# Performance work log

Measured on AMD Instinct MI355X. Metric: run time of the kernel, lower is better.

## Reference

```python
import jax, jax.numpy as jnp
import numpy as np

B_, T_, D_MODEL = 2, 1024, 1024
D_STATE, D_CONV, EXPAND = 16, 4, 2
D_INNER = D_MODEL * EXPAND


def setup_inputs() -> dict:
    key = jax.random.key(0)
    ks = jax.random.split(key, 12)
    def s(k, shape, sc=0.02):
        return jax.random.normal(k, shape, jnp.float32) * sc
    return {
        "x": jax.random.normal(ks[0], (B_, T_, D_MODEL), jnp.float32),
        "ln_g": jnp.ones((D_MODEL,), jnp.float32),
        "ln_b": jnp.zeros((D_MODEL,), jnp.float32),
        "W_in": s(ks[1], (D_MODEL, 2 * D_INNER)),
        "b_in": s(ks[2], (2 * D_INNER,)),
        "conv_w": s(ks[3], (D_INNER, 1, D_CONV)),  # depthwise kernel, torch OIH layout
        "conv_b": s(ks[4], (D_INNER,)),
        "A": s(ks[5], (D_INNER, D_STATE), 0.1),
        "W_B": s(ks[6], (D_INNER, D_STATE)),
        "b_B": s(ks[7], (D_STATE,)),
        "W_C": s(ks[8], (D_INNER, D_STATE)),
        "b_C": s(ks[9], (D_STATE,)),
        "D": jnp.ones((D_INNER,), jnp.float32),
        "W_out": s(ks[10], (D_INNER, D_MODEL)),
        "b_out": s(ks[11], (D_MODEL,)),
    }


def _ssm_forward(x, ln_g, ln_b, W_in, b_in, conv_w, conv_b, A, W_B, b_B, W_C, b_C, D, W_out, b_out):
    eps = 1e-5
    # LayerNorm (biased variance, as in torch)
    mu = jnp.mean(x, axis=-1, keepdims=True)
    var = jnp.var(x, axis=-1, keepdims=True)
    xn = (x - mu) / jnp.sqrt(var + eps) * ln_g + ln_b
    # in_proj -> split into x path and gate
    proj = xn @ W_in + b_in                      # (b, t, 2*d_inner)
    xp, gate = jnp.split(proj, 2, axis=-1)
    # depthwise causal conv1d (padding=d_conv-1 on the left == torch pad + truncate)
    xc = jax.lax.conv_general_dilated(
        xp.transpose(0, 2, 1), conv_w,
        window_strides=(1,), padding=[(D_CONV - 1, 0)],
        dimension_numbers=("NCH", "OIH", "NCH"),
        feature_group_count=D_INNER,
    ).transpose(0, 2, 1) + conv_b                # (b, t, d_inner)
    xc = jax.nn.silu(xc)
    Bt = xc @ W_B + b_B                          # (b, t, d_state)
    Ct = xc @ W_C + b_C                          # (b, t, d_state)
    a = jax.nn.sigmoid(A)                        # (d_inner, d_state), per-channel decay
    u = Bt[:, :, None, :] * xc[:, :, :, None]    # (b, t, d_inner, d_state)
    a_full = jnp.broadcast_to(a, u.shape)
    # h_t = a * h_{t-1} + u_t  via first-order-recurrence associative scan
    def combine(c1, c2):
        a1, u1 = c1
        a2, u2 = c2
        return a2 * a1, a2 * u1 + u2
    _, h = jax.lax.associative_scan(combine, (a_full, u), axis=1)
    y = jnp.einsum("btns,bts->btn", h, Ct) + D * xc
    y = y * jax.nn.silu(gate)
    return y @ W_out + b_out + x                 # residual (dropout is identity in eval)


def reference(x, ln_g, ln_b, W_in, b_in, conv_w, conv_b, A, W_B, b_B, W_C, b_C, D, W_out, b_out):
    return _ssm_forward(x, ln_g, ln_b, W_in, b_in, conv_w, conv_b, A, W_B, b_B, W_C, b_C, D, W_out, b_out)
```

## Files before the change

kernel.cpp:

```cpp
#include <hip/hip_runtime.h>
#include <hip/hip_bf16.h>
#include <stdint.h>

using u16 = unsigned short;
typedef short bf16x8 __attribute__((ext_vector_type(8)));
typedef float f32x4 __attribute__((ext_vector_type(4)));

__device__ __forceinline__ float b2f(u16 u) {
  union { unsigned int i; float f; } v; v.i = ((unsigned int)u) << 16; return v.f;
}
__device__ __forceinline__ u16 f2b(float f) {
  __hip_bfloat16 h = __float2bfloat16(f);
  u16 r; __builtin_memcpy(&r, &h, 2); return r;
}
__device__ __forceinline__ bool probe_bf16(const void* p) {
  return *(const unsigned int*)p == 0x3F803F80u;
}
__device__ __forceinline__ float loadf(const void* p, size_t i, bool bf) {
  return bf ? b2f(((const u16*)p)[i]) : ((const float*)p)[i];
}
__device__ __forceinline__ void gload_lds16(const u16* g, u16* l) {
  __builtin_amdgcn_global_load_lds(
      (const __attribute__((address_space(1))) unsigned int*)(g),
      (__attribute__((address_space(3))) unsigned int*)(l),
      16, 0, 0);
}
template <int BK>
__device__ __forceinline__ int swkey(int row) {
  if constexpr (BK == 32) return (row >> 1) & 3;
  else return row & (BK / 8 - 1);
}

__device__ __forceinline__ void do_transpose(const void* __restrict__ in, u16* __restrict__ out,
                                             int R, int C, int bx, int by, int tid, bool bf) {
  __shared__ u16 tile[32][33];
  int c0 = bx * 32, r0 = by * 32;
  int tx = tid & 31, ty = tid >> 5;
#pragma unroll
  for (int i = 0; i < 4; i++) {
    size_t idx = (size_t)(r0 + ty + i * 8) * C + c0 + tx;
    tile[ty + i * 8][tx] = bf ? ((const u16*)in)[idx] : f2b(((const float*)in)[idx]);
  }
  __syncthreads();
#pragma unroll
  for (int i = 0; i < 4; i++)
    out[(size_t)(c0 + ty + i * 8) * R + r0 + tx] = tile[tx][ty + i * 8];
}

__launch_bounds__(256)
__global__ void prep_kernel(const void* __restrict__ W_in, u16* __restrict__ WinT,
                            const void* __restrict__ W_out, u16* __restrict__ WoutT,
                            const void* __restrict__ WB, const void* __restrict__ WC,
                            u16* __restrict__ WTbc, const void* __restrict__ probe) {
  const bool bf = probe_bf16(probe);
  const int bid = blockIdx.x, tid = threadIdx.x;
  if (bid < 4096) {
    do_transpose(W_in, WinT, 1024, 4096, bid & 127, bid >> 7, tid, bf);
  } else if (bid < 6144) {
    int b2 = bid - 4096;
    do_transpose(W_out, WoutT, 2048, 1024, b2 & 31, b2 >> 5, tid, bf);
  } else {
    int g = (bid - 6144) * 256 + tid;
    int c = g >> 8, k0 = (g & 255) * 8;
    const void* W = (c < 16) ? WB : WC;
    int cc = c & 15;
    u16 pk[8];
#pragma unroll
    for (int e = 0; e < 8; e++)
      pk[e] = bf ? ((const u16*)W)[(size_t)(k0 + e) * 16 + cc]
                 : f2b(((const float*)W)[(size_t)(k0 + e) * 16 + cc]);
    *(int4*)(WTbc + (size_t)c * 2048 + k0) = *(int4*)pk;
  }
}

__launch_bounds__(256)
__global__ void ln_kernel(const void* __restrict__ x, const void* __restrict__ g,
                          const void* __restrict__ b, u16* __restrict__ xn) {
  const bool bf = probe_bf16(g);
  const int row = blockIdx.x, tid = threadIdx.x;
  const size_t base = (size_t)row * 1024;
  float v[4]; float s = 0.f, s2 = 0.f;
#pragma unroll
  for (int i = 0; i < 4; i++) {
    v[i] = loadf(x, base + tid + i * 256, bf);
    s += v[i]; s2 += v[i] * v[i];
  }
#pragma unroll
  for (int m = 32; m >= 1; m >>= 1) { s += __shfl_xor(s, m); s2 += __shfl_xor(s2, m); }
  __shared__ float rs[4], rs2[4];
  if ((tid & 63) == 0) { rs[tid >> 6] = s; rs2[tid >> 6] = s2; }
  __syncthreads();
  s = rs[0] + rs[1] + rs[2] + rs[3];
  s2 = rs2[0] + rs2[1] + rs2[2] + rs2[3];
  float mu = s * (1.f / 1024.f);
  float var = s2 * (1.f / 1024.f) - mu * mu;
  float rstd = rsqrtf(var + 1e-5f);
#pragma unroll
  for (int i = 0; i < 4; i++) {
    int c = tid + i * 256;
    float o = (v[i] - mu) * rstd * loadf(g, c, bf) + loadf(b, c, bf);
    xn[base + c] = f2b(o);
  }
}

template <int ROWS, int BK>
__device__ __forceinline__ void stage_tile(const u16* __restrict__ g, u16* lbuf,
                                           int K, int wave, int lane) {
  constexpr int LPR = BK / 8;
  constexpr int RPI = 512 / BK;
  constexpr int NI = ROWS / RPI;
  const int lr = lane / LPR, lc = lane % LPR;
#pragma unroll
  for (int j = wave; j < NI; j += 4) {
    int row = j * RPI + lr;
    int col = (lc ^ swkey<BK>(row)) * 8;
    gload_lds16(g + (size_t)row * K + col, lbuf + (size_t)j * RPI * BK);
  }
}

template <int BM, int BN, int BK, bool RESID, bool DUALOUT, bool PARTIAL>
__launch_bounds__(256)
__global__ void gemm_async(const u16* __restrict__ A, const u16* __restrict__ BT,
                           const void* __restrict__ bias, const void* __restrict__ resid,
                           void* __restrict__ Cout, float* __restrict__ Cpart,
                           int M, int N, int K, int k_len,
                           const void* __restrict__ probe) {
  constexpr int WM = BM / 2, WN = BN / 2;
  constexpr int TM = WM / 16, TN = WN / 16;
  constexpr int KF = BK / 32;
  __shared__ __align__(16) u16 lds[2][(BM + BN) * BK];
  const int tid = threadIdx.x;
  const int bm = blockIdx.x, bn = blockIdx.y, bz = blockIdx.z;
  const int lane = tid & 63, wave = tid >> 6;
  const int wm = wave >> 1, wn = wave & 1;
  const int lrow = lane & 15, quad = lane >> 4;
  f32x4 acc[TM][TN] = {};
  const u16* Ag = A + (size_t)bm * BM * K + (size_t)bz * k_len;
  const u16* Bg = BT + (size_t)bn * BN * K + (size_t)bz * k_len;

  stage_tile<BM, BK>(Ag, &lds[0][0], K, wave, lane);
  stage_tile<BN, BK>(Bg, &lds[0][BM * BK], K, wave, lane);
  __syncthreads();

  int cur = 0;
  for (int k0 = 0; k0 < k_len; k0 += BK, cur ^= 1) {
    if (k0 + BK < k_len) {
      stage_tile<BM, BK>(Ag + k0 + BK, &lds[cur ^ 1][0], K, wave, lane);
      stage_tile<BN, BK>(Bg + k0 + BK, &lds[cur ^ 1][BM * BK], K, wave, lane);
    }
    const u16* bufA = &lds[cur][0];
    const u16* bufB = &lds[cur][BM * BK];
#pragma unroll
    for (int f = 0; f < KF; f++) {
      bf16x8 af[TM], bv[TN];
#pragma unroll
      for (int i = 0; i < TM; i++) {
        int row = wm * WM + i * 16 + lrow;
        af[i] = *(const bf16x8*)&bufA[(size_t)row * BK + (((f * 4 + quad) ^ swkey<BK>(row)) * 8)];
      }
#pragma unroll
      for (int j = 0; j < TN; j++) {
        int row = wn * WN + j * 16 + lrow;
        bv[j] = *(const bf16x8*)&bufB[(size_t)row * BK + (((f * 4 + quad) ^ swkey<BK>(row)) * 8)];
      }
#pragma unroll
      for (int i = 0; i < TM; i++)
#pragma unroll
        for (int j = 0; j < TN; j++)
          acc[i][j] = __builtin_amdgcn_mfma_f32_16x16x32_bf16(af[i], bv[j], acc[i][j], 0, 0, 0);
    }
    __syncthreads();
  }

  if constexpr (PARTIAL) {
    float* P = Cpart + (size_t)bz * M * N;
#pragma unroll
    for (int i = 0; i < TM; i++)
#pragma unroll
      for (int j = 0; j < TN; j++) {
        int col = bn * BN + wn * WN + j * 16 + lrow;
#pragma unroll
        for (int r = 0; r < 4; r++) {
          int row = bm * BM + wm * WM + i * 16 + quad * 4 + r;
          P[(size_t)row * N + col] = acc[i][j][r];
        }
      }
    return;
  }

  const bool bf = probe_bf16(probe);
#pragma unroll
  for (int i = 0; i < TM; i++) {
#pragma unroll
    for (int j = 0; j < TN; j++) {
      int col = bn * BN + wn * WN + j * 16 + lrow;
      float bvv = loadf(bias, col, bf);
#pragma unroll
      for (int r = 0; r < 4; r++) {
        int row = bm * BM + wm * WM + i * 16 + quad * 4 + r;
        float v = acc[i][j][r] + bvv;
        if constexpr (RESID) v += loadf(resid, (size_t)row * N + col, bf);
        if constexpr (DUALOUT) {
          if (bf) ((u16*)Cout)[(size_t)row * N + col] = f2b(v);
          else    ((float*)Cout)[(size_t)row * N + col] = v;
        } else {
          ((u16*)Cout)[(size_t)row * N + col] = f2b(v);
        }
      }
    }
  }
}

__launch_bounds__(256)
__global__ void reduce_out(const float* __restrict__ p, const void* __restrict__ bias,
                           const void* __restrict__ resid, void* __restrict__ out,
                           const void* __restrict__ probe) {
  const bool bf = probe_bf16(probe);
  const int row = blockIdx.x, c0 = threadIdx.x * 4;
  const size_t i = (size_t)row * 1024 + c0;
  f32x4 a = *(const f32x4*)(p + i);
  f32x4 b = *(const f32x4*)(p + (size_t)2048 * 1024 + i);
  float o[4];
#pragma unroll
  for (int e = 0; e < 4; e++)
    o[e] = a[e] + b[e] + loadf(bias, c0 + e, bf) + loadf(resid, i + e, bf);
  if (bf) {
    u16 pk[4];
#pragma unroll
    for (int e = 0; e < 4; e++) pk[e] = f2b(o[e]);
    *(uint2*)((u16*)out + i) = *(uint2*)pk;
  } else {
    f32x4 v; v[0] = o[0]; v[1] = o[1]; v[2] = o[2]; v[3] = o[3];
    *(f32x4*)((float*)out + i) = v;
  }
}

__global__ void conv_silu_kernel(const u16* __restrict__ proj, const void* __restrict__ cw,
                                 const void* __restrict__ cb, u16* __restrict__ xc,
                                 const void* __restrict__ probe) {
  const bool bf = probe_bf16(probe);
  const int n = blockIdx.x * 256 + threadIdx.x;
  const int row = blockIdx.y;
  const int t = row & 1023;
  float w[4];
#pragma unroll
  for (int k = 0; k < 4; k++) w[k] = loadf(cw, n * 4 + k, bf);
  float s = loadf(cb, n, bf);
#pragma unroll
  for (int k = 0; k < 4; k++) {
    int tt = t - 3 + k;
    if (tt >= 0) s += b2f(proj[(size_t)(row - 3 + k) * 4096 + n]) * w[k];
  }
  float sg = 1.f / (1.f + __expf(-s));
  xc[(size_t)row * 2048 + n] = f2b(s * sg);
}

__launch_bounds__(256)
__global__ void gemm_bc(const u16* __restrict__ A, const u16* __restrict__ WT,
                        float* __restrict__ part) {
  constexpr int BK = 64, KLEN = 128;
  __shared__ __align__(16) u16 lds[2][(128 + 32) * BK];
  const int tid = threadIdx.x;
  const int bm = blockIdx.x, bz = blockIdx.y;
  const int lane = tid & 63, wave = tid >> 6;
  const int lrow = lane & 15, quad = lane >> 4;
  f32x4 acc[2][2] = {};
  const u16* Ag = A + (size_t)bm * 128 * 2048 + bz * KLEN;
  const u16* Bg = WT + bz * KLEN;

  stage_tile<128, BK>(Ag, &lds[0][0], 2048, wave, lane);
  stage_tile<32, BK>(Bg, &lds[0][128 * BK], 2048, wave, lane);
  __syncthreads();
  int cur = 0;
  for (int k0 = 0; k0 < KLEN; k0 += BK, cur ^= 1) {
    if (k0 + BK < KLEN) {
      stage_tile<128, BK>(Ag + k0 + BK, &lds[cur ^ 1][0], 2048, wave, lane);
      stage_tile<32, BK>(Bg + k0 + BK, &lds[cur ^ 1][128 * BK], 2048, wave, lane);
    }
    const u16* bufA = &lds[cur][0];
    const u16* bufB = &lds[cur][128 * BK];
#pragma unroll
    for (int f = 0; f < 2; f++) {
      bf16x8 af[2], bv[2];
#pragma unroll
      for (int i = 0; i < 2; i++) {
        int row = wave * 32 + i * 16 + lrow;
        af[i] = *(const bf16x8*)&bufA[(size_t)row * BK + (((f * 4 + quad) ^ (row & 7)) * 8)];
      }
#pragma unroll
      for (int j = 0; j < 2; j++) {
        int row = j * 16 + lrow;
        bv[j] = *(const bf16x8*)&bufB[(size_t)row * BK + (((f * 4 + quad) ^ (row & 7)) * 8)];
      }
#pragma unroll
      for (int i = 0; i < 2; i++)
#pragma unroll
        for (int j = 0; j < 2; j++)
          acc[i][j] = __builtin_amdgcn_mfma_f32_16x16x32_bf16(af[i], bv[j], acc[i][j], 0, 0, 0);
    }
    __syncthreads();
  }
#pragma unroll
  for (int i = 0; i < 2; i++)
#pragma unroll
    for (int j = 0; j < 2; j++) {
      int col = j * 16 + lrow;
#pragma unroll
      for (int r = 0; r < 4; r++) {
        int row = bm * 128 + wave * 32 + i * 16 + quad * 4 + r;
        part[((size_t)bz * 2048 + row) * 32 + col] = acc[i][j][r];
      }
    }
}

__launch_bounds__(256)
__global__ void reduce_bc(const float* __restrict__ part, const void* __restrict__ bB,
                          const void* __restrict__ bC, float* __restrict__ BC,
                          const void* __restrict__ probe) {
  const bool bf = probe_bf16(probe);
  const int g = blockIdx.x * 256 + threadIdx.x;
  const int c = g & 31;
  float s = (c < 16) ? loadf(bB, c, bf) : loadf(bC, c - 16, bf);
#pragma unroll
  for (int z = 0; z < 16; z++) s += part[(size_t)z * 65536 + g];
  BC[g] = s;
}

__launch_bounds__(256)
__global__ void scan_pass1(const u16* __restrict__ xc, const float* __restrict__ BC,
                           const void* __restrict__ Abuf, float* __restrict__ carry,
                           const void* __restrict__ probe) {
  const bool bf = probe_bf16(probe);
  const int tid = threadIdx.x;
  const int c = blockIdx.x & 31, ng = (blockIdx.x >> 5) & 7, bi = blockIdx.x >> 8;
  const int n = ng * 256 + tid;
  float a[16], h[16];
#pragma unroll
  for (int s = 0; s < 16; s++) {
    float av = loadf(Abuf, n * 16 + s, bf);
    a[s] = 1.f / (1.f + __expf(-av));
    h[s] = 0.f;
  }
  __shared__ __align__(16) u16 xs[32 * 256];
  __shared__ __align__(16) float bcs[32 * 32];
  const u16* xcp = xc + (size_t)bi * 1024 * 2048 + ng * 256;
  const float* bcp = BC + (size_t)bi * 1024 * 32;
  const int tc = c * 32;
#pragma unroll
  for (int i = 0; i < 4; i++) {
    int ch = tid + i * 256;
    int r = ch >> 5, cv = (ch & 31) * 8;
    *(int4*)&xs[ch * 8] = *(const int4*)(xcp + (size_t)(tc + r) * 2048 + cv);
  }
  {
    int r = tid >> 3, cv = (tid & 7) * 4;
    *(int4*)&bcs[tid * 4] = *(const int4*)(bcp + (size_t)(tc + r) * 32 + cv);
  }
  __syncthreads();
  for (int t = 0; t < 32; t++) {
    float x = b2f(xs[t * 256 + tid]);
#pragma unroll
    for (int s = 0; s < 16; s++)
      h[s] = __builtin_fmaf(a[s], h[s], bcs[t * 32 + s] * x);
  }
  float* cp = carry + ((size_t)(bi * 32 + c) * 2048 + n) * 16;
#pragma unroll
  for (int s = 0; s < 16; s++) cp[s] = h[s];
}

__launch_bounds__(256)
__global__ void scan_prefix(float* __restrict__ carry, const void* __restrict__ Abuf,
                            const void* __restrict__ probe) {
  const bool bf = probe_bf16(probe);
  const int g = blockIdx.x * 256 + threadIdx.x;
  const int s = g & 15, n = (g >> 4) & 2047, bi = g >> 15;
  float a = 1.f / (1.f + __expf(-loadf(Abuf, n * 16 + s, bf)));
  float aL = a;
#pragma unroll
  for (int i = 0; i < 5; i++) aL = aL * aL;
  float running = 0.f;
  for (int c = 0; c < 32; c++) {
    size_t idx = ((size_t)(bi * 32 + c) * 2048 + n) * 16 + s;
    float tmp = carry[idx];
    carry[idx] = running;
    running = __builtin_fmaf(aL, running, tmp);
  }
}

__launch_bounds__(256)
__global__ void scan_pass2(const u16* __restrict__ xc, const u16* __restrict__ proj,
                           const float* __restrict__ BC, const void* __restrict__ Abuf,
                           const void* __restrict__ Dbuf, const float* __restrict__ carry,
                           u16* __restrict__ ybar, const void* __restrict__ probe) {
  const bool bf = probe_bf16(probe);
  const int tid = threadIdx.x;
  const int c = blockIdx.x & 31, ng = (blockIdx.x >> 5) & 7, bi = blockIdx.x >> 8;
  const int n = ng * 256 + tid;
  float a[16], h[16];
  const float* cp = carry + ((size_t)(bi * 32 + c) * 2048 + n) * 16;
#pragma unroll
  for (int s = 0; s < 16; s++) {
    float av = loadf(Abuf, n * 16 + s, bf);
    a[s] = 1.f / (1.f + __expf(-av));
    h[s] = cp[s];
  }
  const float Dn = loadf(Dbuf, n, bf);
  __shared__ __align__(16) u16 xs[32 * 256];
  __shared__ __align__(16) u16 gs[32 * 256];
  __shared__ __align__(16) float bcs[32 * 32];
  const u16* xcp = xc + (size_t)bi * 1024 * 2048 + ng * 256;
  const u16* gp = proj + (size_t)bi * 1024 * 4096 + 2048 + ng * 256;
  const float* bcp = BC + (size_t)bi * 1024 * 32;
  u16* yp = ybar + (size_t)bi * 1024 * 2048 + ng * 256;
  const int tc = c * 32;
#pragma unroll
  for (int i = 0; i < 4; i++) {
    int ch = tid + i * 256;
    int r = ch >> 5, cv = (ch & 31) * 8;
    *(int4*)&xs[ch * 8] = *(const int4*)(xcp + (size_t)(tc + r) * 2048 + cv);
    *(int4*)&gs[ch * 8] = *(const int4*)(gp + (size_t)(tc + r) * 4096 + cv);
  }
  {
    int r = tid >> 3, cv = (tid & 7) * 4;
    *(int4*)&bcs[tid * 4] = *(const int4*)(bcp + (size_t)(tc + r) * 32 + cv);
  }
  __syncthreads();
  for (int t = 0; t < 32; t++) {
    float x = b2f(xs[t * 256 + tid]);
    float acc = 0.f;
#pragma unroll
    for (int s = 0; s < 16; s++) {
      h[s] = __builtin_fmaf(a[s], h[s], bcs[t * 32 + s] * x);
      acc = __builtin_fmaf(h[s], bcs[t * 32 + 16 + s], acc);
    }
    float y = acc + Dn * x;
    float g = b2f(gs[t * 256 + tid]);
    float yg = y * g / (1.f + __expf(-g));
    yp[(size_t)(tc + t) * 2048 + tid] = f2b(yg);
  }
}

extern "C" void kernel_launch(void* const* d_in, const int* in_sizes, int n_in,
                              void* d_out, int out_size, void* d_ws, size_t ws_size,
                              hipStream_t stream) {
  const void* x = d_in[0];
  const void* ln_g = d_in[1];
  const void* ln_b = d_in[2];
  const void* W_in = d_in[3];
  const void* b_in = d_in[4];
  const void* conv_w = d_in[5];
  const void* conv_b = d_in[6];
  const void* A = d_in[7];
  const void* W_B = d_in[8];
  const void* b_B = d_in[9];
  const void* W_C = d_in[10];
  const void* b_C = d_in[11];
  const void* Dp = d_in[12];
  const void* W_out = d_in[13];
  const void* b_out = d_in[14];
  const void* probe = ln_g;

  char* ws = (char*)d_ws;
  u16* WinT = (u16*)ws;
  u16* ybar = (u16*)ws;
  u16* xn = (u16*)(ws + (size_t)8 * 1024 * 1024);
  u16* proj = (u16*)(ws + (size_t)12 * 1024 * 1024);
  u16* xcb = (u16*)(ws + (size_t)28 * 1024 * 1024);
  float* BC = (float*)(ws + (size_t)36 * 1024 * 1024);
  float* carry = (float*)(ws + (size_t)36 * 1024 * 1024 + 256 * 1024);
  u16* WTbc = (u16*)(ws + (size_t)46 * 1024 * 1024);
  float* part = (float*)(ws + (size_t)48 * 1024 * 1024);
  u16* WoutT = (u16*)(ws + (size_t)64 * 1024 * 1024);
  float* part_bc = (float*)(ws + (size_t)68 * 1024 * 1024);

  prep_kernel<<<6176, 256, 0, stream>>>(W_in, WinT, W_out, WoutT, W_B, W_C, WTbc, probe);
  ln_kernel<<<2048, 256, 0, stream>>>(x, ln_g, ln_b, xn);
  gemm_async<128, 128, 64, false, false, false><<<dim3(16, 32), 256, 0, stream>>>(
      xn, WinT, b_in, nullptr, proj, nullptr, 2048, 4096, 1024, 1024, probe);
  conv_silu_kernel<<<dim3(8, 2048), 256, 0, stream>>>(proj, conv_w, conv_b, xcb, probe);
  gemm_bc<<<dim3(16, 16), 256, 0, stream>>>(xcb, WTbc, part_bc);
  reduce_bc<<<256, 256, 0, stream>>>(part_bc, b_B, b_C, BC, probe);
  scan_pass1<<<512, 256, 0, stream>>>(xcb, BC, A, carry, probe);
  scan_prefix<<<256, 256, 0, stream>>>(carry, A, probe);
  scan_pass2<<<512, 256, 0, stream>>>(xcb, proj, BC, A, Dp, carry, ybar, probe);
  gemm_async<128, 64, 64, false, false, true><<<dim3(16, 16, 2), 256, 0, stream>>>(
      ybar, WoutT, nullptr, nullptr, nullptr, part, 2048, 1024, 2048, 1024, probe);
  reduce_out<<<2048, 256, 0, stream>>>(part, b_out, x, d_out, probe);
}
```

Baseline: 219.3 us.

## Fuse LN into prep, conv into BC GEMM, and scan passes into cooperative kernel

Merges the LayerNorm launch into the weight-prep kernel. The depthwise conv+SiLU is computed inside the B/C projection GEMM, writing xc while also staging it into LDS for the MFMA. The BC partial reduction and the three scan phases (chunk carry, prefix, output) are folded into one cooperative kernel that uses grid-wide syncs. This removes several launches and some global round trips, in exchange for grid-sync overhead and needing all 512 blocks to be co-resident.

Result: slower. 466.9 us (+112.9%).

```diff
diff --git a/kernel.cpp b/kernel.cpp
--- a/kernel.cpp
+++ b/kernel.cpp
@@ -1,6 +1,9 @@
 #include <hip/hip_runtime.h>
 #include <hip/hip_bf16.h>
+#include <hip/hip_cooperative_groups.h>
 #include <stdint.h>
+
+namespace cg = cooperative_groups;
 
 using u16 = unsigned short;
 typedef short bf16x8 __attribute__((ext_vector_type(8)));
@@ -48,20 +51,22 @@
 }
 
 __launch_bounds__(256)
-__global__ void prep_kernel(const void* __restrict__ W_in, u16* __restrict__ WinT,
-                            const void* __restrict__ W_out, u16* __restrict__ WoutT,
-                            const void* __restrict__ WB, const void* __restrict__ WC,
-                            u16* __restrict__ WTbc, const void* __restrict__ probe) {
-  const bool bf = probe_bf16(probe);
+__global__ void prep_ln_kernel(const void* __restrict__ W_in, u16* __restrict__ WinT,
+                               const void* __restrict__ W_out, u16* __restrict__ WoutT,
+                               const void* __restrict__ WB, const void* __restrict__ WC,
+                               u16* __restrict__ WTbc, const void* __restrict__ x,
+                               const void* __restrict__ g, const void* __restrict__ b,
+                               u16* __restrict__ xn) {
+  const bool bf = probe_bf16(g);
   const int bid = blockIdx.x, tid = threadIdx.x;
   if (bid < 4096) {
     do_transpose(W_in, WinT, 1024, 4096, bid & 127, bid >> 7, tid, bf);
   } else if (bid < 6144) {
     int b2 = bid - 4096;
     do_transpose(W_out, WoutT, 2048, 1024, b2 & 31, b2 >> 5, tid, bf);
-  } else {
-    int g = (bid - 6144) * 256 + tid;
-    int c = g >> 8, k0 = (g & 255) * 8;
+  } else if (bid < 6176) {
+    int gg = (bid - 6144) * 256 + tid;
+    int c = gg >> 8, k0 = (gg & 255) * 8;
     const void* W = (c < 16) ? WB : WC;
     int cc = c & 15;
     u16 pk[8];
@@ -70,36 +75,31 @@
       pk[e] = bf ? ((const u16*)W)[(size_t)(k0 + e) * 16 + cc]
                  : f2b(((const float*)W)[(size_t)(k0 + e) * 16 + cc]);
     *(int4*)(WTbc + (size_t)c * 2048 + k0) = *(int4*)pk;
-  }
-}
-
-__launch_bounds__(256)
-__global__ void ln_kernel(const void* __restrict__ x, const void* __restrict__ g,
-                          const void* __restrict__ b, u16* __restrict__ xn) {
-  const bool bf = probe_bf16(g);
-  const int row = blockIdx.x, tid = threadIdx.x;
-  const size_t base = (size_t)row * 1024;
-  float v[4]; float s = 0.f, s2 = 0.f;
-#pragma unroll
-  for (int i = 0; i < 4; i++) {
-    v[i] = loadf(x, base + tid + i * 256, bf);
-    s += v[i]; s2 += v[i] * v[i];
-  }
-#pragma unroll
-  for (int m = 32; m >= 1; m >>= 1) { s += __shfl_xor(s, m); s2 += __shfl_xor(s2, m); }
-  __shared__ float rs[4], rs2[4];
-  if ((tid & 63) == 0) { rs[tid >> 6] = s; rs2[tid >> 6] = s2; }
-  __syncthreads();
-  s = rs[0] + rs[1] + rs[2] + rs[3];
-  s2 = rs2[0] + rs2[1] + rs2[2] + rs2[3];
-  float mu = s * (1.f / 1024.f);
-  float var = s2 * (1.f / 1024.f) - mu * mu;
-  float rstd = rsqrtf(var + 1e-5f);
-#pragma unroll
-  for (int i = 0; i < 4; i++) {
-    int c = tid + i * 256;
-    float o = (v[i] - mu) * rstd * loadf(g, c, bf) + loadf(b, c, bf);
-    xn[base + c] = f2b(o);
+  } else {
+    const int row = bid - 6176;
+    const size_t base = (size_t)row * 1024;
+    float v[4]; float s = 0.f, s2 = 0.f;
+#pragma unroll
+    for (int i = 0; i < 4; i++) {
+      v[i] = loadf(x, base + tid + i * 256, bf);
+      s += v[i]; s2 += v[i] * v[i];
+    }
+#pragma unroll
+    for (int m = 32; m >= 1; m >>= 1) { s += __shfl_xor(s, m); s2 += __shfl_xor(s2, m); }
+    __shared__ float rs[4], rs2[4];
+    if ((tid & 63) == 0) { rs[tid >> 6] = s; rs2[tid >> 6] = s2; }
+    __syncthreads();
+    s = rs[0] + rs[1] + rs[2] + rs[3];
+    s2 = rs2[0] + rs2[1] + rs2[2] + rs2[3];
+    float mu = s * (1.f / 1024.f);
+    float var = s2 * (1.f / 1024.f) - mu * mu;
+    float rstd = rsqrtf(var + 1e-5f);
+#pragma unroll
+    for (int i = 0; i < 4; i++) {
+      int c = tid + i * 256;
+      float o = (v[i] - mu) * rstd * loadf(g, c, bf) + loadf(b, c, bf);
+      xn[base + c] = f2b(o);
+    }
   }
 }
 
@@ -118,12 +118,11 @@
   }
 }
 
-template <int BM, int BN, int BK, bool RESID, bool DUALOUT, bool PARTIAL>
+template <int BM, int BN, int BK, bool PARTIAL>
 __launch_bounds__(256)
 __global__ void gemm_async(const u16* __restrict__ A, const u16* __restrict__ BT,
-                           const void* __restrict__ bias, const void* __restrict__ resid,
-                           void* __restrict__ Cout, float* __restrict__ Cpart,
-                           int M, int N, int K, int k_len,
+                           const void* __restrict__ bias, void* __restrict__ Cout,
+                           float* __restrict__ Cpart, int M, int N, int K, int k_len,
                            const void* __restrict__ probe) {
   constexpr int WM = BM / 2, WN = BN / 2;
   constexpr int TM = WM / 16, TN = WN / 16;
@@ -198,14 +197,7 @@
 #pragma unroll
       for (int r = 0; r < 4; r++) {
         int row = bm * BM + wm * WM + i * 16 + quad * 4 + r;
-        float v = acc[i][j][r] + bvv;
-        if constexpr (RESID) v += loadf(resid, (size_t)row * N + col, bf);
-        if constexpr (DUALOUT) {
-          if (bf) ((u16*)Cout)[(size_t)row * N + col] = f2b(v);
-          else    ((float*)Cout)[(size_t)row * N + col] = v;
-        } else {
-          ((u16*)Cout)[(size_t)row * N + col] = f2b(v);
-        }
+        ((u16*)Cout)[(size_t)row * N + col] = f2b(acc[i][j][r] + bvv);
       }
     }
   }
@@ -235,70 +227,79 @@
   }
 }
 
-__global__ void conv_silu_kernel(const u16* __restrict__ proj, const void* __restrict__ cw,
-                                 const void* __restrict__ cb, u16* __restrict__ xc,
-                                 const void* __restrict__ probe) {
+__launch_bounds__(256)
+__global__ void gemm_bc_conv(const u16* __restrict__ proj, const void* __restrict__ cw,
+                             const void* __restrict__ cb, const u16* __restrict__ WT,
+                             u16* __restrict__ xcb, float* __restrict__ part,
+                             const void* __restrict__ probe) {
   const bool bf = probe_bf16(probe);
-  const int n = blockIdx.x * 256 + threadIdx.x;
-  const int row = blockIdx.y;
-  const int t = row & 1023;
-  float w[4];
-#pragma unroll
-  for (int k = 0; k < 4; k++) w[k] = loadf(cw, n * 4 + k, bf);
-  float s = loadf(cb, n, bf);
-#pragma unroll
-  for (int k = 0; k < 4; k++) {
-    int tt = t - 3 + k;
-    if (tt >= 0) s += b2f(proj[(size_t)(row - 3 + k) * 4096 + n]) * w[k];
-  }
-  float sg = 1.f / (1.f + __expf(-s));
-  xc[(size_t)row * 2048 + n] = f2b(s * sg);
-}
-
-__launch_bounds__(256)
-__global__ void gemm_bc(const u16* __restrict__ A, const u16* __restrict__ WT,
-                        float* __restrict__ part) {
-  constexpr int BK = 64, KLEN = 128;
-  __shared__ __align__(16) u16 lds[2][(128 + 32) * BK];
+  __shared__ __align__(16) u16 lA[128 * 128];
+  __shared__ __align__(16) u16 lB[32 * 128];
   const int tid = threadIdx.x;
   const int bm = blockIdx.x, bz = blockIdx.y;
   const int lane = tid & 63, wave = tid >> 6;
   const int lrow = lane & 15, quad = lane >> 4;
+
+  stage_tile<32, 128>(WT + bz * 128, lB, 2048, wave, lane);
+
+  const int kb = tid & 15;
+  const int ch0 = bz * 128 + kb * 8;
+  float wgt[8][4], bia[8];
+#pragma unroll
+  for (int e = 0; e < 8; e++) {
+    bia[e] = loadf(cb, ch0 + e, bf);
+#pragma unroll
+    for (int k = 0; k < 4; k++) wgt[e][k] = loadf(cw, (size_t)(ch0 + e) * 4 + k, bf);
+  }
+#pragma unroll
+  for (int i = 0; i < 8; i++) {
+    int slot = tid + i * 256;
+    int r = slot >> 4;
+    int grow = bm * 128 + r;
+    int t = grow & 1023;
+    float acc[8];
+#pragma unroll
+    for (int e = 0; e < 8; e++) acc[e] = bia[e];
+#pragma unroll
+    for (int k = 0; k < 4; k++) {
+      if (t - 3 + k >= 0) {
+        union { int4 v; u16 u[8]; } uu;
+        uu.v = *(const int4*)(proj + (size_t)(grow - 3 + k) * 4096 + ch0);
+#pragma unroll
+        for (int e = 0; e < 8; e++)
+          acc[e] = __builtin_fmaf(b2f(uu.u[e]), wgt[e][k], acc[e]);
+      }
+    }
+    union { int4 v; u16 u[8]; } pk;
+#pragma unroll
+    for (int e = 0; e < 8; e++) {
+      float s = acc[e];
+      pk.u[e] = f2b(s / (1.f + __expf(-s)));
+    }
+    *(int4*)(xcb + (size_t)grow * 2048 + ch0) = pk.v;
+    *(int4*)&lA[r * 128 + ((kb ^ (r & 15)) * 8)] = pk.v;
+  }
+  __syncthreads();
+
   f32x4 acc[2][2] = {};
-  const u16* Ag = A + (size_t)bm * 128 * 2048 + bz * KLEN;
-  const u16* Bg = WT + bz * KLEN;
-
-  stage_tile<128, BK>(Ag, &lds[0][0], 2048, wave, lane);
-  stage_tile<32, BK>(Bg, &lds[0][128 * BK], 2048, wave, lane);
-  __syncthreads();
-  int cur = 0;
-  for (int k0 = 0; k0 < KLEN; k0 += BK, cur ^= 1) {
-    if (k0 + BK < KLEN) {
-      stage_tile<128, BK>(Ag + k0 + BK, &lds[cur ^ 1][0], 2048, wave, lane);
-      stage_tile<32, BK>(Bg + k0 + BK, &lds[cur ^ 1][128 * BK], 2048, wave, lane);
-    }
-    const u16* bufA = &lds[cur][0];
-    const u16* bufB = &lds[cur][128 * BK];
-#pragma unroll
-    for (int f = 0; f < 2; f++) {
-      bf16x8 af[2], bv[2];
-#pragma unroll
-      for (int i = 0; i < 2; i++) {
-        int row = wave * 32 + i * 16 + lrow;
-        af[i] = *(const bf16x8*)&bufA[(size_t)row * BK + (((f * 4 + quad) ^ (row & 7)) * 8)];
-      }
-#pragma unroll
-      for (int j = 0; j < 2; j++) {
-        int row = j * 16 + lrow;
-        bv[j] = *(const bf16x8*)&bufB[(size_t)row * BK + (((f * 4 + quad) ^ (row & 7)) * 8)];
-      }
-#pragma unroll
-      for (int i = 0; i < 2; i++)
-#pragma unroll
-        for (int j = 0; j < 2; j++)
-          acc[i][j] = __builtin_amdgcn_mfma_f32_16x16x32_bf16(af[i], bv[j], acc[i][j], 0, 0, 0);
-    }
-    __syncthreads();
+#pragma unroll
+  for (int f = 0; f < 4; f++) {
+    bf16x8 af[2], bv[2];
+#pragma unroll
+    for (int i = 0; i < 2; i++) {
+      int row = wave * 32 + i * 16 + lrow;
+      af[i] = *(const bf16x8*)&lA[(size_t)row * 128 + (((f * 4 + quad) ^ (row & 15)) * 8)];
+    }
+#pragma unroll
+    for (int j = 0; j < 2; j++) {
+      int row = j * 16 + lrow;
+      bv[j] = *(const bf16x8*)&lB[(size_t)row * 128 + (((f * 4 + quad) ^ (row & 15)) * 8)];
+    }
+#pragma unroll
+    for (int i = 0; i < 2; i++)
+#pragma unroll
+      for (int j = 0; j < 2; j++)
+        acc[i][j] = __builtin_amdgcn_mfma_f32_16x16x32_bf16(af[i], bv[j], acc[i][j], 0, 0, 0);
   }
 #pragma unroll
   for (int i = 0; i < 2; i++)
@@ -314,105 +315,35 @@
 }
 
 __launch_bounds__(256)
-__global__ void reduce_bc(const float* __restrict__ part, const void* __restrict__ bB,
-                          const void* __restrict__ bC, float* __restrict__ BC,
-                          const void* __restrict__ probe) {
-  const bool bf = probe_bf16(probe);
-  const int g = blockIdx.x * 256 + threadIdx.x;
-  const int c = g & 31;
-  float s = (c < 16) ? loadf(bB, c, bf) : loadf(bC, c - 16, bf);
-#pragma unroll
-  for (int z = 0; z < 16; z++) s += part[(size_t)z * 65536 + g];
-  BC[g] = s;
-}
-
-__launch_bounds__(256)
-__global__ void scan_pass1(const u16* __restrict__ xc, const float* __restrict__ BC,
-                           const void* __restrict__ Abuf, float* __restrict__ carry,
-                           const void* __restrict__ probe) {
-  const bool bf = probe_bf16(probe);
-  const int tid = threadIdx.x;
-  const int c = blockIdx.x & 31, ng = (blockIdx.x >> 5) & 7, bi = blockIdx.x >> 8;
-  const int n = ng * 256 + tid;
-  float a[16], h[16];
-#pragma unroll
-  for (int s = 0; s < 16; s++) {
-    float av = loadf(Abuf, n * 16 + s, bf);
-    a[s] = 1.f / (1.f + __expf(-av));
-    h[s] = 0.f;
-  }
-  __shared__ __align__(16) u16 xs[32 * 256];
-  __shared__ __align__(16) float bcs[32 * 32];
-  const u16* xcp = xc + (size_t)bi * 1024 * 2048 + ng * 256;
-  const float* bcp = BC + (size_t)bi * 1024 * 32;
-  const int tc = c * 32;
-#pragma unroll
-  for (int i = 0; i < 4; i++) {
-    int ch = tid + i * 256;
-    int r = ch >> 5, cv = (ch & 31) * 8;
-    *(int4*)&xs[ch * 8] = *(const int4*)(xcp + (size_t)(tc + r) * 2048 + cv);
-  }
-  {
-    int r = tid >> 3, cv = (tid & 7) * 4;
-    *(int4*)&bcs[tid * 4] = *(const int4*)(bcp + (size_t)(tc + r) * 32 + cv);
-  }
-  __syncthreads();
-  for (int t = 0; t < 32; t++) {
-    float x = b2f(xs[t * 256 + tid]);
-#pragma unroll
-    for (int s = 0; s < 16; s++)
-      h[s] = __builtin_fmaf(a[s], h[s], bcs[t * 32 + s] * x);
-  }
-  float* cp = carry + ((size_t)(bi * 32 + c) * 2048 + n) * 16;
-#pragma unroll
-  for (int s = 0; s < 16; s++) cp[s] = h[s];
-}
-
-__launch_bounds__(256)
-__global__ void scan_prefix(float* __restrict__ carry, const void* __restrict__ Abuf,
-                            const void* __restrict__ probe) {
-  const bool bf = probe_bf16(probe);
-  const int g = blockIdx.x * 256 + threadIdx.x;
-  const int s = g & 15, n = (g >> 4) & 2047, bi = g >> 15;
-  float a = 1.f / (1.f + __expf(-loadf(Abuf, n * 16 + s, bf)));
-  float aL = a;
-#pragma unroll
-  for (int i = 0; i < 5; i++) aL = aL * aL;
-  float running = 0.f;
-  for (int c = 0; c < 32; c++) {
-    size_t idx = ((size_t)(bi * 32 + c) * 2048 + n) * 16 + s;
-    float tmp = carry[idx];
-    carry[idx] = running;
-    running = __builtin_fmaf(aL, running, tmp);
-  }
-}
-
-__launch_bounds__(256)
-__global__ void scan_pass2(const u16* __restrict__ xc, const u16* __restrict__ proj,
-                           const float* __restrict__ BC, const void* __restrict__ Abuf,
-                           const void* __restrict__ Dbuf, const float* __restrict__ carry,
+__global__ void scan_fused(const u16* __restrict__ xc, const u16* __restrict__ proj,
+                           const float* __restrict__ part_bc, const void* __restrict__ bB,
+                           const void* __restrict__ bC, const void* __restrict__ Abuf,
+                           const void* __restrict__ Dbuf, float* __restrict__ carry,
                            u16* __restrict__ ybar, const void* __restrict__ probe) {
   const bool bf = probe_bf16(probe);
   const int tid = threadIdx.x;
-  const int c = blockIdx.x & 31, ng = (blockIdx.x >> 5) & 7, bi = blockIdx.x >> 8;
+  const int bk = blockIdx.x;
+  const int c = bk & 31, ng = (bk >> 5) & 7, bi = bk >> 8;
   const int n = ng * 256 + tid;
-  float a[16], h[16];
-  const float* cp = carry + ((size_t)(bi * 32 + c) * 2048 + n) * 16;
-#pragma unroll
-  for (int s = 0; s < 16; s++) {
-    float av = loadf(Abuf, n * 16 + s, bf);
-    a[s] = 1.f / (1.f + __expf(-av));
-    h[s] = cp[s];
-  }
-  const float Dn = loadf(Dbuf, n, bf);
+  const int tc = c * 32;
+
   __shared__ __align__(16) u16 xs[32 * 256];
   __shared__ __align__(16) u16 gs[32 * 256];
   __shared__ __align__(16) float bcs[32 * 32];
+
+#pragma unroll
+  for (int e = 0; e < 4; e++) {
+    int idx = tid * 4 + e;
+    int tt = idx >> 5, cc = idx & 31;
+    size_t grow = (size_t)bi * 1024 + tc + tt;
+    float s = (cc < 16) ? loadf(bB, cc, bf) : loadf(bC, cc - 16, bf);
+#pragma unroll
+    for (int z = 0; z < 16; z++) s += part_bc[(size_t)z * 65536 + grow * 32 + cc];
+    bcs[idx] = s;
+  }
+
   const u16* xcp = xc + (size_t)bi * 1024 * 2048 + ng * 256;
   const u16* gp = proj + (size_t)bi * 1024 * 4096 + 2048 + ng * 256;
-  const float* bcp = BC + (size_t)bi * 1024 * 32;
-  u16* yp = ybar + (size_t)bi * 1024 * 2048 + ng * 256;
-  const int tc = c * 32;
 #pragma unroll
   for (int i = 0; i < 4; i++) {
     int ch = tid + i * 256;
@@ -420,11 +351,57 @@
     *(int4*)&xs[ch * 8] = *(const int4*)(xcp + (size_t)(tc + r) * 2048 + cv);
     *(int4*)&gs[ch * 8] = *(const int4*)(gp + (size_t)(tc + r) * 4096 + cv);
   }
+
+  float a[16], h[16];
+#pragma unroll
+  for (int s = 0; s < 16; s++) {
+    float av = loadf(Abuf, n * 16 + s, bf);
+    a[s] = 1.f / (1.f + __expf(-av));
+    h[s] = 0.f;
+  }
+  __syncthreads();
+
+  for (int t = 0; t < 32; t++) {
+    float x = b2f(xs[t * 256 + tid]);
+#pragma unroll
+    for (int s = 0; s < 16; s++)
+      h[s] = __builtin_fmaf(a[s], h[s], bcs[t * 32 + s] * x);
+  }
   {
-    int r = tid >> 3, cv = (tid & 7) * 4;
-    *(int4*)&bcs[tid * 4] = *(const int4*)(bcp + (size_t)(tc + r) * 32 + cv);
-  }
-  __syncthreads();
+    float* cp = carry + ((size_t)(bi * 32 + c) * 2048 + n) * 16;
+#pragma unroll
+    for (int s = 0; s < 16; s++) cp[s] = h[s];
+  }
+  __threadfence();
+  cg::this_grid().sync();
+
+  {
+    int gid = bk * 256 + tid;
+    if (gid < 65536) {
+      int ps = gid & 15, pn = (gid >> 4) & 2047, pbi = gid >> 15;
+      float pa = 1.f / (1.f + __expf(-loadf(Abuf, pn * 16 + ps, bf)));
+      float aL = pa;
+#pragma unroll
+      for (int i = 0; i < 5; i++) aL = aL * aL;
+      float running = 0.f;
+      for (int cc = 0; cc < 32; cc++) {
+        size_t idx = ((size_t)(pbi * 32 + cc) * 2048 + pn) * 16 + ps;
+        float tmp = carry[idx];
+        carry[idx] = running;
+        running = __builtin_fmaf(aL, running, tmp);
+      }
+    }
+  }
+  __threadfence();
+  cg::this_grid().sync();
+
+  {
+    const float* cp = carry + ((size_t)(bi * 32 + c) * 2048 + n) * 16;
+#pragma unroll
+    for (int s = 0; s < 16; s++) h[s] = cp[s];
+  }
+  const float Dn = loadf(Dbuf, n, bf);
+  u16* yp = ybar + (size_t)bi * 1024 * 2048 + ng * 256;
   for (int t = 0; t < 32; t++) {
     float x = b2f(xs[t * 256 + tid]);
     float acc = 0.f;
@@ -466,24 +443,28 @@
   u16* xn = (u16*)(ws + (size_t)8 * 1024 * 1024);
   u16* proj = (u16*)(ws + (size_t)12 * 1024 * 1024);
   u16* xcb = (u16*)(ws + (size_t)28 * 1024 * 1024);
-  float* BC = (float*)(ws + (size_t)36 * 1024 * 1024);
   float* carry = (float*)(ws + (size_t)36 * 1024 * 1024 + 256 * 1024);
   u16* WTbc = (u16*)(ws + (size_t)46 * 1024 * 1024);
   float* part = (float*)(ws + (size_t)48 * 1024 * 1024);
   u16* WoutT = (u16*)(ws + (size_t)64 * 1024 * 1024);
   float* part_bc = (float*)(ws + (size_t)68 * 1024 * 1024);
 
-  prep_kernel<<<6176, 256, 0, stream>>>(W_in, WinT, W_out, WoutT, W_B, W_C, WTbc, probe);
-  ln_kernel<<<2048, 256, 0, stream>>>(x, ln_g, ln_b, xn);
-  gemm_async<128, 128, 64, false, false, false><<<dim3(16, 32), 256, 0, stream>>>(
-      xn, WinT, b_in, nullptr, proj, nullptr, 2048, 4096, 1024, 1024, probe);
-  conv_silu_kernel<<<dim3(8, 2048), 256, 0, stream>>>(proj, conv_w, conv_b, xcb, probe);
-  gemm_bc<<<dim3(16, 16), 256, 0, stream>>>(xcb, WTbc, part_bc);
-  reduce_bc<<<256, 256, 0, stream>>>(part_bc, b_B, b_C, BC, probe);
-  scan_pass1<<<512, 256, 0, stream>>>(xcb, BC, A, carry, probe);
-  scan_prefix<<<256, 256, 0, stream>>>(carry, A, probe);
-  scan_pass2<<<512, 256, 0, stream>>>(xcb, proj, BC, A, Dp, carry, ybar, probe);
-  gemm_async<128, 64, 64, false, false, true><<<dim3(16, 16, 2), 256, 0, stream>>>(
-      ybar, WoutT, nullptr, nullptr, nullptr, part, 2048, 1024, 2048, 1024, probe);
+  prep_ln_kernel<<<8224, 256, 0, stream>>>(W_in, WinT, W_out, WoutT, W_B, W_C, WTbc,
+                                           x, ln_g, ln_b, xn);
+  gemm_async<128, 128, 64, false><<<dim3(16, 32), 256, 0, stream>>>(
+      xn, WinT, b_in, proj, nullptr, 2048, 4096, 1024, 1024, probe);
+  gemm_bc_conv<<<dim3(16, 16), 256, 0, stream>>>(proj, conv_w, conv_b, WTbc,
+                                                 xcb, part_bc, probe);
+  {
+    void* xc_p = (void*)xcb; void* proj_p = (void*)proj; void* pbc_p = (void*)part_bc;
+    void* bB_p = (void*)b_B; void* bC_p = (void*)b_C; void* A_p = (void*)A;
+    void* D_p = (void*)Dp; void* carry_p = (void*)carry; void* ybar_p = (void*)ybar;
+    void* probe_p = (void*)probe;
+    void* args[] = {&xc_p, &proj_p, &pbc_p, &bB_p, &bC_p, &A_p, &D_p,
+                    &carry_p, &ybar_p, &probe_p};
+    hipLaunchCooperativeKernel((void*)scan_fused, dim3(512), dim3(256), args, 0, stream);
+  }
+  gemm_async<128, 64, 64, true><<<dim3(16, 16, 2), 256, 0, stream>>>(
+      ybar, WoutT, nullptr, nullptr, part, 2048, 1024, 2048, 1024, probe);
   reduce_out<<<2048, 256, 0, stream>>>(part, b_out, x, d_out, probe);
 }
```
